# Kernel tuning notes

Hardware: AMD Instinct MI355X
Metric: run time of the kernel (lower is better)

Reference implementation:

```python
import jax, jax.numpy as jnp
import numpy as np

IMG = 224   # img_size
K = 8       # num_bands
E = 256     # embed_dim


def _radial_masks(size, k):
    # Faithful to torch _create_radial_masks: center = size//2, max_r = size/sqrt(2)
    center = size // 2
    y, x = jnp.meshgrid(jnp.arange(size), jnp.arange(size), indexing='ij')
    r = jnp.sqrt(((x - center) ** 2 + (y - center) ** 2).astype(jnp.float32))
    max_r = size / np.sqrt(2.0)
    step = np.float32(max_r / k)
    i = jnp.arange(k, dtype=jnp.float32)[:, None, None]
    masks = ((r[None] >= step * i) & (r[None] < step * (i + 1.0))).astype(jnp.float32)
    return masks  # [K, H, W]


def setup_inputs() -> dict:
    key = jax.random.key(0)
    ks = jax.random.split(key, 3)
    x = jax.random.normal(ks[0], (64, 3, IMG, IMG), dtype=jnp.float32)
    W1 = jax.random.normal(ks[1], (3, E), dtype=jnp.float32) * 0.3
    b1 = jnp.zeros((E,), jnp.float32)
    gamma = jnp.ones((E,), jnp.float32)
    beta = jnp.zeros((E,), jnp.float32)
    W2 = jax.random.normal(ks[2], (E, E), dtype=jnp.float32) * (1.0 / np.sqrt(E))
    b2 = jnp.zeros((E,), jnp.float32)
    return {"x": x, "W1": W1, "b1": b1, "gamma": gamma, "beta": beta, "W2": W2, "b2": b2}


def reference(x, W1, b1, gamma, beta, W2, b2):
    masks = _radial_masks(IMG, K)                    # [K,H,W], binary, non-overlapping
    x_gray = x.mean(axis=1)                          # [B,H,W]
    fft = jnp.fft.fftshift(jnp.fft.fft2(x_gray), axes=(-2, -1))
    mag = jnp.log1p(jnp.abs(fft))                    # log(1+|F|)
    mu = mag.mean(axis=(1, 2), keepdims=True)
    sd = jnp.std(mag, axis=(1, 2), keepdims=True, ddof=1) + 1e-6  # torch .std is unbiased
    magn = (mag - mu) / sd                           # [B,H,W]

    msum = masks.sum(axis=(1, 2))                    # [K], true mask pixel counts
    mask_sums = msum + 1e-6
    s1 = jnp.einsum('bhw,khw->bk', magn, masks)      # per-band sum
    s2 = jnp.einsum('bhw,khw->bk', magn * magn, masks)
    means = s1 / mask_sums
    # sum((magn - means)^2 * mask) = s2 - 2*means*s1 + means^2 * msum  (exact expansion)
    var_num = s2 - 2.0 * means * s1 + (means ** 2) * msum
    stds = jnp.sqrt(var_num / mask_sums + 1e-6)
    # masked_fill(mask==0, -1e9) then amax over H,W
    maxs = jnp.max(jnp.where(masks[None] > 0, magn[:, None], -1e9), axis=(2, 3))

    feats = jnp.stack([means, stds, maxs], axis=-1)  # [B,K,3]
    h = feats @ W1 + b1                              # [B,K,E]
    hm = h.mean(axis=-1, keepdims=True)
    hv = h.var(axis=-1, keepdims=True)
    h = (h - hm) / jnp.sqrt(hv + 1e-5) * gamma + beta  # LayerNorm, eps=1e-5
    h = jax.nn.relu(h)
    return h @ W2 + b2                               # [B,K,E]
```

## Files before the change

kernel.cpp:

```cpp
#include <hip/hip_runtime.h>
#include <math.h>

#define IMG 224
#define NPIX 50176
#define BATCH 64
#define EDIM 256

typedef _Float16 f16;
typedef __attribute__((ext_vector_type(8))) _Float16 f16x8;
typedef __attribute__((ext_vector_type(4))) _Float16 f16x4;
typedef __attribute__((ext_vector_type(4))) float f32x4;
typedef unsigned int u32;


#define GLD16(gp, lp)                                                          \
  __builtin_amdgcn_global_load_lds(                                            \
      (const __attribute__((address_space(1))) u32*)(gp),                      \
      (__attribute__((address_space(3))) u32*)(lp), 16, 0, 0)

__global__ __launch_bounds__(256) void gemmA_kernel(const float* __restrict__ x,
                                                    f16* __restrict__ B2t,
                                                    f16* __restrict__ W2h,
                                                    u32* __restrict__ statsz) {
  __shared__ float T[224];
  __shared__ f16 As[2][32][64];
  __shared__ f16 Bs[2][256][64];
  int m0 = blockIdx.x * 32;
  int tid = threadIdx.x;
  int lane = tid & 63, wid = tid >> 6;

  if (blockIdx.x == 0) {
#pragma unroll
    for (int i = 0; i < 9; ++i) {
      int idx = i * 256 + tid;
      if (idx < 2176) statsz[idx] = 0u;
    }
  }

  int arow = tid >> 3;
  int aseg = tid & 7;
  int am = m0 + arow;
  int ab = am / 224, ah = am - ab * 224;
  const float* px = x + (size_t)ab * 3 * NPIX + ah * IMG;
  int s0 = aseg ^ (arow & 7);

  f32x4 xlA[3][2], xlB[3][2];
  f32x4 acc[2][4];
#pragma unroll
  for (int i = 0; i < 2; ++i)
#pragma unroll
    for (int j = 0; j < 4; ++j) acc[i][j] = (f32x4){0.f, 0.f, 0.f, 0.f};

  auto issueA = [&](f32x4 (&xl)[3][2], int t) {
    int kb = t * 64 + aseg * 8;
    if (kb < 224) {
#pragma unroll
      for (int c = 0; c < 3; ++c) {
        xl[c][0] = *(const f32x4*)(px + c * NPIX + kb);
        xl[c][1] = *(const f32x4*)(px + c * NPIX + kb + 4);
      }
    }
  };
  auto writeA = [&](f32x4 (&xl)[3][2], int t, int bufi) {
    int kb = t * 64 + aseg * 8;
    f16x8 h0;
    if (kb < 224) {
#pragma unroll
      for (int j = 0; j < 8; ++j) {
        int q = j >> 2, r = j & 3;
        h0[j] = (f16)((xl[0][q][r] + xl[1][q][r] + xl[2][q][r]) * (1.0f / 3.0f));
      }
    } else {
#pragma unroll
      for (int j = 0; j < 8; ++j) h0[j] = (f16)0.f;
    }
    *(f16x8*)&As[bufi][arow][s0 * 8] = h0;
  };
  auto computeB = [&](int bufi, int t) {
    int row = tid;
    int v = (row < 113) ? row : row - 113;
    u32 off = (row < 113) ? 0u : 56u;
    u32 idx0 = ((u32)(t * 64) * (u32)v + off) % 224u;
    u32 idxm = (idx0 >= (u32)v) ? idx0 - (u32)v : idx0 + 224u - (u32)v;
    float cur = T[idx0];
    float prev = T[idxm];
    float k2c = 2.0f * T[v];
#pragma unroll
    for (int g = 0; g < 8; ++g) {
      f16x8 hv;
#pragma unroll
      for (int j = 0; j < 8; ++j) {
        hv[j] = (f16)cur;
        float nxt = __builtin_fmaf(k2c, cur, -prev);
        prev = cur; cur = nxt;
      }
      *(f16x8*)&Bs[bufi][row][(g ^ (row & 7)) * 8] = hv;
    }
  };
  auto mfmaStep = [&](int bufi) {
#pragma unroll
    for (int kk = 0; kk < 2; ++kk) {
      f16x8 af[2], bfr[4];
#pragma unroll
      for (int mi = 0; mi < 2; ++mi) {
        int row = mi * 16 + (lane & 15);
        int slot = (kk * 4 + (lane >> 4)) ^ (row & 7);
        af[mi] = *(const f16x8*)&As[bufi][row][slot * 8];
      }
#pragma unroll
      for (int nj = 0; nj < 4; ++nj) {
        int row = wid * 64 + nj * 16 + (lane & 15);
        int slot = (kk * 4 + (lane >> 4)) ^ (row & 7);
        bfr[nj] = *(const f16x8*)&Bs[bufi][row][slot * 8];
      }
#pragma unroll
      for (int mi = 0; mi < 2; ++mi)
#pragma unroll
        for (int nj = 0; nj < 4; ++nj)
          acc[mi][nj] = __builtin_amdgcn_mfma_f32_16x16x32_f16(
              af[mi], bfr[nj], acc[mi][nj], 0, 0, 0);
    }
  };

  issueA(xlA, 0);
  if (tid < 224) T[tid] = cospif((float)tid / 112.0f);
  issueA(xlB, 1);
  __syncthreads();
  computeB(0, 0);

  asm volatile("s_waitcnt vmcnt(6)" ::: "memory");
  writeA(xlA, 0, 0);
  asm volatile("s_waitcnt lgkmcnt(0)" ::: "memory");
  __builtin_amdgcn_s_barrier();
  issueA(xlA, 2);
  computeB(1, 1);
  mfmaStep(0);
  __builtin_amdgcn_s_barrier();
  asm volatile("s_waitcnt vmcnt(6)" ::: "memory");
  writeA(xlB, 1, 1);
  asm volatile("s_waitcnt lgkmcnt(0)" ::: "memory");
  __builtin_amdgcn_s_barrier();
  issueA(xlB, 3);
  computeB(0, 2);
  mfmaStep(1);
  __builtin_amdgcn_s_barrier();
  asm volatile("s_waitcnt vmcnt(6)" ::: "memory");
  writeA(xlA, 2, 0);
  asm volatile("s_waitcnt lgkmcnt(0)" ::: "memory");
  __builtin_amdgcn_s_barrier();
  computeB(1, 3);
  mfmaStep(0);
  __builtin_amdgcn_s_barrier();
  asm volatile("s_waitcnt vmcnt(0)" ::: "memory");
  writeA(xlB, 3, 1);
  asm volatile("s_waitcnt lgkmcnt(0)" ::: "memory");
  __builtin_amdgcn_s_barrier();
  mfmaStep(1);

  int nbase = wid * 64;
#pragma unroll
  for (int mi = 0; mi < 2; ++mi) {
#pragma unroll
    for (int nj = 0; nj < 4; ++nj) {
      int c = nbase + nj * 16 + (lane & 15);
      if (c >= 226) continue;
      int m = m0 + mi * 16 + ((lane >> 4) << 2);
      int b = m / 224;
      int h = m - b * 224;
      int v = c, kb = h;
      if (c >= 113) { v = c - 113; kb = 224 + h; }
      size_t off = (size_t)(b * 128 + v) * 448 + kb;
      f32x4 y = acc[mi][nj];
      f16x4 hv;
#pragma unroll
      for (int r = 0; r < 4; ++r) hv[r] = (f16)y[r];
      *(f16x4*)&B2t[off] = hv;
    }
  }

  {
    int r = blockIdx.x;
    int u = r >> 1;
    bool imrow = r & 1;
#pragma unroll
    for (int pass = 0; pass < 2; ++pass) {
      int k = pass * 256 + tid;
      if (k < 448) {
        bool kim = k >= 224;
        int kk = kim ? k - 224 : k;
        int m = (u * kk) % 224;
        float mf = (float)m / 112.0f;
        float c = cospif(mf), s = sinpif(mf);
        float val = imrow ? (kim ? c : -s) : (kim ? s : c);
        W2h[(size_t)r * 448 + k] = (f16)val;
      }
    }
  }
}

__global__ __launch_bounds__(256) void gemmB_kernel(const f16* __restrict__ W2h,
                                                    const f16* __restrict__ B2t,
                                                    float* __restrict__ stats) {
  __shared__ f16 As[64][64];
  __shared__ f16 Bs[128][64];
  int b = blockIdx.x;
  int m0 = blockIdx.y * 64;
  int tid = threadIdx.x;
  int lane = tid & 63, wid = tid >> 6;
  int wr = wid >> 1, wc = wid & 1;
  const f16* Ap = W2h + (size_t)m0 * 448;
  const f16* Bp = B2t + (size_t)b * 128 * 448;

  int srow = lane >> 3;
  int sk8 = (lane & 7) ^ srow;

  f32x4 acc[2][4];
#pragma unroll
  for (int i = 0; i < 2; ++i)
#pragma unroll
    for (int j = 0; j < 4; ++j) acc[i][j] = (f32x4){0.f, 0.f, 0.f, 0.f};

#pragma unroll 1
  for (int t = 0; t < 7; ++t) {
    int k0 = t * 64;
#pragma unroll
    for (int ci = 0; ci < 6; ++ci) {
      int c = wid * 6 + ci;
      if (c < 8) {
        GLD16(Ap + (size_t)(c * 8 + srow) * 448 + k0 + sk8 * 8,
              &As[0][0] + c * 512);
      } else {
        int j = c - 8;
        GLD16(Bp + (size_t)(j * 8 + srow) * 448 + k0 + sk8 * 8,
              &Bs[0][0] + j * 512);
      }
    }
    __syncthreads();
#pragma unroll
    for (int kk = 0; kk < 2; ++kk) {
      f16x8 af[2], bfr[4];
#pragma unroll
      for (int mi = 0; mi < 2; ++mi) {
        int row = wr * 32 + mi * 16 + (lane & 15);
        int slot = (kk * 4 + (lane >> 4)) ^ (row & 7);
        af[mi] = *(const f16x8*)&As[row][slot * 8];
      }
#pragma unroll
      for (int nj = 0; nj < 4; ++nj) {
        int row = wc * 64 + nj * 16 + (lane & 15);
        int slot = (kk * 4 + (lane >> 4)) ^ (row & 7);
        bfr[nj] = *(const f16x8*)&Bs[row][slot * 8];
      }
#pragma unroll
      for (int mi = 0; mi < 2; ++mi)
#pragma unroll
        for (int nj = 0; nj < 4; ++nj)
          acc[mi][nj] = __builtin_amdgcn_mfma_f32_16x16x32_f16(
              af[mi], bfr[nj], acc[mi][nj], 0, 0, 0);
    }
    __syncthreads();
  }

  int rbase = m0 + wr * 32;
  const float step = (float)(158.39191898578665 / 8.0);
  float gsum = 0.f, gsq = 0.f;
  float s1[8] = {0}, s2[8] = {0}, cnt[8] = {0};
  float mx[8] = {0, 0, 0, 0, 0, 0, 0, 0};

#pragma unroll
  for (int mi = 0; mi < 2; ++mi) {
#pragma unroll
    for (int nj = 0; nj < 4; ++nj) {
      int n = wc * 64 + nj * 16 + (lane & 15);
      if (n >= 113) continue;
      float wgt = (n >= 1 && n <= 111) ? 2.f : 1.f;
      float dx2 = (float)(n * n);
      int rr = rbase + mi * 16 + ((lane >> 4) << 2);
      f32x4 f = acc[mi][nj];
#pragma unroll
      for (int p = 0; p < 2; ++p) {
        int u = (rr >> 1) + p;
        float re = f[2 * p], im = f[2 * p + 1];
        float mv = log1pf(sqrtf(re * re + im * im));
        int a = (u <= 111) ? u : 224 - u;
        float r = sqrtf((float)(a * a) + dx2);
        int bd = 255;
#pragma unroll
        for (int k = 0; k < 8; k++) {
          float lo = step * (float)k;
          float hi = step * (float)(k + 1);
          if (r >= lo && r < hi) bd = k;
        }
        float wm = wgt * mv;
        gsum += wm;
        gsq += wm * mv;
#pragma unroll
        for (int k = 0; k < 8; k++) {
          bool m = (bd == k);
          s1[k] += m ? wm : 0.f;
          s2[k] += m ? wm * mv : 0.f;
          cnt[k] += m ? wgt : 0.f;
          mx[k] = m ? fmaxf(mx[k], mv) : mx[k];
        }
      }
    }
  }

  float vals[34];
  vals[0] = gsum; vals[1] = gsq;
#pragma unroll
  for (int k = 0; k < 8; k++) {
    vals[2 + k] = s1[k]; vals[10 + k] = s2[k]; vals[18 + k] = mx[k]; vals[26 + k] = cnt[k];
  }
#pragma unroll
  for (int i = 0; i < 34; i++) {
    float v = vals[i];
    const bool isMax = (i >= 18 && i < 26);
#pragma unroll
    for (int off = 32; off > 0; off >>= 1) {
      float o = __shfl_down(v, off);
      v = isMax ? fmaxf(v, o) : (v + o);
    }
    vals[i] = v;
  }
  float* red = (float*)&As[0][0];
  if ((tid & 63) == 0) {
#pragma unroll
    for (int i = 0; i < 34; i++) red[wid * 34 + i] = vals[i];
  }
  __syncthreads();
  if (tid < 34) {
    bool isMax = (tid >= 18 && tid < 26);
    float v = red[tid];
#pragma unroll
    for (int ww = 1; ww < 4; ww++) {
      float o = red[ww * 34 + tid];
      v = isMax ? fmaxf(v, o) : (v + o);
    }
    if (isMax)
      atomicMax((u32*)&stats[b * 34 + tid], __float_as_uint(v));
    else
      atomicAdd(&stats[b * 34 + tid], v);
  }
}

__global__ __launch_bounds__(256) void mlp_kernel(const float* __restrict__ stats,
                                                  const float* __restrict__ W1,
                                                  const float* __restrict__ b1,
                                                  const float* __restrict__ gamma,
                                                  const float* __restrict__ beta,
                                                  const float* __restrict__ W2m,
                                                  const float* __restrict__ b2,
                                                  float* __restrict__ out) {
  int blk = blockIdx.x;
  int b = blk >> 2;
  int k0 = (blk & 3) * 2;
  int e = threadIdx.x;
  int lane = e & 63, wave = e >> 6;

  __shared__ float st[34];
  if (e < 34) st[e] = stats[b * 34 + e];
  __syncthreads();

  const float N = (float)NPIX;
  float mu = st[0] / N;
  float varg = fmaxf(st[1] - N * mu * mu, 0.0f) / (N - 1.0f);
  float sd = sqrtf(varg) + 1e-6f;

  float g_e = gamma[e], bt_e = beta[e], b1_e = b1[e];
  float w1a = W1[e], w1b = W1[EDIM + e], w1c = W1[2 * EDIM + e];

  float h[2];
#pragma unroll
  for (int q = 0; q < 2; ++q) {
    int k = k0 + q;
    float s1r = st[2 + k], s2r = st[10 + k], mxr = st[18 + k], cntk = st[26 + k];
    float ms = cntk + 1e-6f;
    float s1n = (s1r - mu * cntk) / sd;
    float s2n = (s2r - 2.0f * mu * s1r + mu * mu * cntk) / (sd * sd);
    float mean_k = s1n / ms;
    float var_num = s2n - 2.0f * mean_k * s1n + mean_k * mean_k * cntk;
    float std_k = sqrtf(var_num / ms + 1e-6f);
    float max_k = (mxr - mu) / sd;
    h[q] = mean_k * w1a + std_k * w1b + max_k * w1c + b1_e;
  }

  float v4[4] = {h[0], h[0] * h[0], h[1], h[1] * h[1]};
#pragma unroll
  for (int i = 0; i < 4; ++i) {
#pragma unroll
    for (int off = 32; off > 0; off >>= 1) v4[i] += __shfl_down(v4[i], off);
  }
  __shared__ float red[4][4];
  __shared__ float mm[4];
  if (lane == 0) {
#pragma unroll
    for (int i = 0; i < 4; ++i) red[wave][i] = v4[i];
  }
  __syncthreads();
  if (e == 0) {
#pragma unroll
    for (int i = 0; i < 4; ++i) {
      float t = red[0][i] + red[1][i] + red[2][i] + red[3][i];
      red[0][i] = t;
    }
    float hm0 = red[0][0] / 256.0f, hm1 = red[0][2] / 256.0f;
    mm[0] = hm0;
    mm[1] = fmaxf(red[0][1] / 256.0f - hm0 * hm0, 0.0f);
    mm[2] = hm1;
    mm[3] = fmaxf(red[0][3] / 256.0f - hm1 * hm1, 0.0f);
  }
  __syncthreads();

  __shared__ float hsT[EDIM][2];
#pragma unroll
  for (int q = 0; q < 2; ++q) {
    float hn = (h[q] - mm[2 * q]) / sqrtf(mm[2 * q + 1] + 1e-5f) * g_e + bt_e;
    hsT[e][q] = fmaxf(hn, 0.0f);
  }
  __syncthreads();

  float a0 = b2[e], a1 = a0;
#pragma unroll 8
  for (int j = 0; j < EDIM; j++) {
    float w = W2m[j * EDIM + e];
    float2 hp = *(const float2*)&hsT[j][0];
    a0 += hp.x * w;
    a1 += hp.y * w;
  }
  out[(size_t)(b * 8 + k0) * EDIM + e] = a0;
  out[(size_t)(b * 8 + k0 + 1) * EDIM + e] = a1;
}

extern "C" void kernel_launch(void* const* d_in, const int* in_sizes, int n_in,
                              void* d_out, int out_size, void* d_ws, size_t ws_size,
                              hipStream_t stream) {
  const float* x     = (const float*)d_in[0];
  const float* W1    = (const float*)d_in[1];
  const float* b1    = (const float*)d_in[2];
  const float* gamma = (const float*)d_in[3];
  const float* beta  = (const float*)d_in[4];
  const float* W2m   = (const float*)d_in[5];
  const float* b2    = (const float*)d_in[6];
  float* out = (float*)d_out;

  char* W = (char*)d_ws;
  f16* B2t = (f16*)W;
  float* stats = (float*)(W + 7340032);
  f16* W2h = (f16*)(W + 7340032 + 8704);

  gemmA_kernel<<<dim3(448), dim3(256), 0, stream>>>(x, B2t, W2h, (u32*)stats);
  gemmB_kernel<<<dim3(BATCH, 7), dim3(256), 0, stream>>>(W2h, B2t, stats);
  mlp_kernel<<<dim3(256), dim3(256), 0, stream>>>(stats, W1, b1, gamma, beta, W2m, b2, out);
}
```

Baseline: 51.24 us.

## Prefetch next K-tile into registers while computing MFMA on current LDS tile

Replaces the direct global-to-LDS loads in the second GEMM kernel with register-staged loads. The loop is fully unrolled over the seven K-steps: each step writes the already-loaded registers to LDS, syncs, issues the global loads for the next tile, then runs the MFMAs. This is meant to hide global load latency behind compute, at the cost of more registers for two staging buffers and an extra LDS write pass through VGPRs.

```diff
diff --git a/kernel.cpp b/kernel.cpp
--- a/kernel.cpp
+++ b/kernel.cpp
@@ -12,11 +12,6 @@
 typedef __attribute__((ext_vector_type(4))) float f32x4;
 typedef unsigned int u32;
 
-
-#define GLD16(gp, lp)                                                          \
-  __builtin_amdgcn_global_load_lds(                                            \
-      (const __attribute__((address_space(1))) u32*)(gp),                      \
-      (__attribute__((address_space(3))) u32*)(lp), 16, 0, 0)
 
 __global__ __launch_bounds__(256) void gemmA_kernel(const float* __restrict__ x,
                                                     f16* __restrict__ B2t,
@@ -220,22 +215,27 @@
 #pragma unroll
     for (int j = 0; j < 4; ++j) acc[i][j] = (f32x4){0.f, 0.f, 0.f, 0.f};
 
-#pragma unroll 1
-  for (int t = 0; t < 7; ++t) {
+  auto stage_load = [&](f16x8 (&tmp)[6], int t) {
     int k0 = t * 64;
 #pragma unroll
     for (int ci = 0; ci < 6; ++ci) {
       int c = wid * 6 + ci;
-      if (c < 8) {
-        GLD16(Ap + (size_t)(c * 8 + srow) * 448 + k0 + sk8 * 8,
-              &As[0][0] + c * 512);
-      } else {
-        int j = c - 8;
-        GLD16(Bp + (size_t)(j * 8 + srow) * 448 + k0 + sk8 * 8,
-              &Bs[0][0] + j * 512);
-      }
-    }
-    __syncthreads();
+      const f16* src = (c < 8)
+          ? Ap + (size_t)(c * 8 + srow) * 448 + k0 + sk8 * 8
+          : Bp + (size_t)((c - 8) * 8 + srow) * 448 + k0 + sk8 * 8;
+      tmp[ci] = *(const f16x8*)src;
+    }
+  };
+  auto stage_write = [&](f16x8 (&tmp)[6]) {
+#pragma unroll
+    for (int ci = 0; ci < 6; ++ci) {
+      int c = wid * 6 + ci;
+      f16* dst = (c < 8) ? (&As[0][0] + c * 512 + lane * 8)
+                         : (&Bs[0][0] + (c - 8) * 512 + lane * 8);
+      *(f16x8*)dst = tmp[ci];
+    }
+  };
+  auto mfmaStep = [&]() {
 #pragma unroll
     for (int kk = 0; kk < 2; ++kk) {
       f16x8 af[2], bfr[4];
@@ -258,11 +258,27 @@
           acc[mi][nj] = __builtin_amdgcn_mfma_f32_16x16x32_f16(
               af[mi], bfr[nj], acc[mi][nj], 0, 0, 0);
     }
+  };
+  auto step = [&](f16x8 (&curT)[6], f16x8 (&nxtT)[6], int t, bool last) {
+    stage_write(curT);
     __syncthreads();
-  }
+    if (!last) stage_load(nxtT, t + 1);
+    mfmaStep();
+    __syncthreads();
+  };
+
+  f16x8 tA[6], tB[6];
+  stage_load(tA, 0);
+  step(tA, tB, 0, false);
+  step(tB, tA, 1, false);
+  step(tA, tB, 2, false);
+  step(tB, tA, 3, false);
+  step(tA, tB, 4, false);
+  step(tB, tA, 5, false);
+  step(tA, tA, 6, true);
 
   int rbase = m0 + wr * 32;
-  const float step = (float)(158.39191898578665 / 8.0);
+  const float step_ = (float)(158.39191898578665 / 8.0);
   float gsum = 0.f, gsq = 0.f;
   float s1[8] = {0}, s2[8] = {0}, cnt[8] = {0};
   float mx[8] = {0, 0, 0, 0, 0, 0, 0, 0};
@@ -287,8 +303,8 @@
         int bd = 255;
 #pragma unroll
         for (int k = 0; k < 8; k++) {
-          float lo = step * (float)k;
-          float hi = step * (float)(k + 1);
+          float lo = step_ * (float)k;
+          float hi = step_ * (float)(k + 1);
           if (r >= lo && r < hi) bd = k;
         }
         float wm = wgt * mv;
```

Result: no change. 50.93 us (-0.6%).
